# Optimization experiments

Measured on AMD Instinct MI355X. Metric: run time of the kernel, lower is better.

## Reference

```python
import jax, jax.numpy as jnp
import numpy as np
from jax import lax

BN_EPS = 1e-5


def _gcn_layer(X, edge_index, W, sW, sb, gamma, beta):
    # X: (B, T, V, Fin). Self-loop linear + per-edge message + scatter-add.
    H = X @ sW + sb  # (B, T, V, Hd)
    src = edge_index[:, 0]
    dst = edge_index[:, 1]
    msgs = X[:, :, src, :] @ W  # (B, T, E, Hd) gather + GEMM
    H = H + jnp.zeros_like(H).at[:, :, dst, :].add(msgs)  # scatter-add over dst
    # BatchNorm1d applied per timestep in the torch loop -> stats over (B, V) per t
    mean = H.mean(axis=(0, 2), keepdims=True)
    var = H.var(axis=(0, 2), keepdims=True)  # biased var, as torch train-mode BN
    H = (H - mean) * lax.rsqrt(var + BN_EPS) * gamma + beta
    return jax.nn.relu(H)


def _conv_bn_relu(x, w, b, gamma, beta, dilation, padding):
    # x: (B, C, T), w: (O, I, K)
    y = lax.conv_general_dilated(x, w, window_strides=(1,),
                                 padding=[(padding, padding)],
                                 rhs_dilation=(dilation,),
                                 dimension_numbers=('NCH', 'OIH', 'NCH'))
    y = y + b[None, :, None]
    mean = y.mean(axis=(0, 2), keepdims=True)
    var = y.var(axis=(0, 2), keepdims=True)
    y = (y - mean) * lax.rsqrt(var + BN_EPS) * gamma[None, :, None] + beta[None, :, None]
    return jax.nn.relu(y)


def setup_inputs() -> dict:
    key = jax.random.key(0)
    ks = jax.random.split(key, 16)
    B, C, T, V, Hd, E, NC = 64, 3, 512, 25, 64, 48, 60
    s = 0.05
    inp = {
        'X': jax.random.normal(ks[0], (B, C, T, V), jnp.float32),
        'edge_index': jax.random.randint(ks[1], (E, 2), 0, V, jnp.int32),
        'W1': jax.random.normal(ks[2], (C, Hd), jnp.float32) * s,
        's1W': jax.random.normal(ks[3], (C, Hd), jnp.float32) * s,
        's1b': jax.random.normal(ks[4], (Hd,), jnp.float32) * s,
        'g1': jnp.ones((Hd,), jnp.float32),
        'b1': jnp.zeros((Hd,), jnp.float32),
        'W2': jax.random.normal(ks[5], (Hd, Hd), jnp.float32) * s,
        's2W': jax.random.normal(ks[6], (Hd, Hd), jnp.float32) * s,
        's2b': jax.random.normal(ks[7], (Hd,), jnp.float32) * s,
        'g2': jnp.ones((Hd,), jnp.float32),
        'b2': jnp.zeros((Hd,), jnp.float32),
        'c1W': jax.random.normal(ks[8], (64, V * Hd, 3), jnp.float32) * s,
        'c1b': jax.random.normal(ks[9], (64,), jnp.float32) * s,
        'tg1': jnp.ones((64,), jnp.float32),
        'tb1': jnp.zeros((64,), jnp.float32),
        'c2W': jax.random.normal(ks[10], (128, 64, 3), jnp.float32) * s,
        'c2b': jax.random.normal(ks[11], (128,), jnp.float32) * s,
        'tg2': jnp.ones((128,), jnp.float32),
        'tb2': jnp.zeros((128,), jnp.float32),
        'fcW': jax.random.normal(ks[12], (128, NC), jnp.float32) * s,
        'fcb': jax.random.normal(ks[13], (NC,), jnp.float32) * s,
    }
    return inp


def reference(X, edge_index, W1, s1W, s1b, g1, b1, W2, s2W, s2b, g2, b2,
              c1W, c1b, tg1, tb1, c2W, c2b, tg2, tb2, fcW, fcb):
    B, C, T, V = X.shape
    Xt = jnp.transpose(X, (0, 2, 3, 1))  # (B, T, V, C)
    H = _gcn_layer(Xt, edge_index, W1, s1W, s1b, g1, b1)  # (B, T, V, Hd)
    H = _gcn_layer(H, edge_index, W2, s2W, s2b, g2, b2)   # (B, T, V, Hd)
    Hd = H.shape[-1]
    # permute(0,2,3,1).reshape(B, V*Hd, T)
    z = jnp.transpose(H, (0, 2, 3, 1)).reshape(B, V * Hd, T)
    z = _conv_bn_relu(z, c1W, c1b, tg1, tb1, dilation=1, padding=1)
    z = _conv_bn_relu(z, c2W, c2b, tg2, tb2, dilation=2, padding=2)
    z = z.mean(axis=2)  # (B, 128)
    return z @ fcW + fcb
```

## Files before the change

### kernel.cpp

```cpp
#include <hip/hip_runtime.h>
#include <hip/hip_bf16.h>
#include <cstddef>

using bf16 = __hip_bfloat16;
typedef __attribute__((ext_vector_type(4)))  short bf16x4;
typedef __attribute__((ext_vector_type(8)))  short bf16x8;
typedef __attribute__((ext_vector_type(4)))  float f32x4;
typedef __attribute__((ext_vector_type(16))) float f32x16;
typedef __attribute__((ext_vector_type(2)))  unsigned int uint32x2;
typedef __attribute__((ext_vector_type(4)))  unsigned int uint32x4;

#define B_   64
#define T_   512
#define V_   25
#define HD_  64
#define E_   48
#define NC_  60

__device__ __forceinline__ bf16  f2b(float x){ return __float2bfloat16(x); }
__device__ __forceinline__ unsigned short f2bits(float x){ return __builtin_bit_cast(unsigned short, f2b(x)); }
__device__ __forceinline__ float bits2f(unsigned short s){ return __builtin_bit_cast(float, ((unsigned)s)<<16); }
__device__ __forceinline__ unsigned cvtpk(float lo, float hi){
  unsigned r;
  asm("v_cvt_pk_bf16_f32 %0, %1, %2" : "=v"(r) : "v"(lo), "v"(hi));
  return r;
}
__device__ __forceinline__ short cvt1(float x){ return (short)(unsigned short)cvtpk(x, x); }

__global__ void k_csr(const int* __restrict__ ei, int* __restrict__ offs, int* __restrict__ lst)
{
  if(threadIdx.x == 0){
    int cnt[V_], pos[V_];
    for(int v=0;v<V_;v++) cnt[v]=0;
    for(int e=0;e<E_;e++) cnt[ei[2*e+1]]++;
    int off = 0;
    for(int v=0;v<V_;v++){ offs[v]=off; pos[v]=off; off+=cnt[v]; }
    offs[V_] = off;
    for(int e=0;e<E_;e++){ int d = ei[2*e+1]; lst[pos[d]++] = ei[2*e+0]; }
  }
}

__global__ void k_wt(const float* __restrict__ c1W, const float* __restrict__ c2W,
                     const float* __restrict__ s2W, const float* __restrict__ W2,
                     const float* __restrict__ s1W, const float* __restrict__ W1,
                     bf16* __restrict__ Wb, bf16* __restrict__ Wb2,
                     bf16* __restrict__ WbB, bf16* __restrict__ W6f)
{
  int i0 = blockIdx.x*blockDim.x + threadIdx.x, stride = gridDim.x*blockDim.x;
  for(int i = i0; i < 307200; i += stride){
    int hlo = i & 15, o = (i>>4)&63, kc = (i>>10)%12, v = i/12288;
    int ks = kc>>2, h = (kc&3)*16 + hlo;
    Wb[i] = f2b(c1W[(o*1600 + v*64 + h)*3 + ks]);
  }
  for(int i = i0; i < 24576; i += stride){
    int hlo = i & 15, o = (i>>4)&127, kc = i>>11;
    int ks = kc>>2, c = (kc&3)*16 + hlo;
    Wb2[i] = f2b(c2W[(o*64 + c)*3 + ks]);
  }
  for(int i = i0; i < 8192; i += stride){
    int j = i&7, l=(i>>3)&63, n=(i>>9)&3, kt=i>>11;
    int k = kt*32 + (l>>4)*8 + j;
    int h = n*16 + (l&15);
    float val = (k < 64) ? s2W[k*64 + h] : W2[(k-64)*64 + h];
    WbB[i] = f2b(val);
  }
  for(int i = i0; i < 2048; i += stride){
    int j = i&7, l=(i>>3)&63, n=(i>>9)&3;
    int k = (l>>4)*8 + j, h = n*16 + (l&15);
    float val = 0.f;
    if(k < 3) val = s1W[k*64 + h];
    else if(k < 6) val = W1[(k-3)*64 + h];
    W6f[i] = f2b(val);
  }
}

__global__ __launch_bounds__(512) void k_gcn1s(
    const float* __restrict__ X, const bf16* __restrict__ W6f,
    const int* __restrict__ offs, const int* __restrict__ lst, float* __restrict__ part)
{
  int tid = threadIdx.x, lane = tid & 63, wid = tid >> 6;
  int b = blockIdx.y, t0 = blockIdx.x*16;
  __shared__ short Z6[3200];
  __shared__ short Xs[1248];
  __shared__ float red[8192];
  __shared__ unsigned char soc[32], slc[48];

  bf16x8 w6[4];
  #pragma unroll
  for(int n=0;n<4;n++) w6[n] = *(const bf16x8*)&W6f[(n*64 + lane)*8];

  if(tid < V_+1) soc[tid] = (unsigned char)offs[tid];
  else if(tid >= 64 && tid < 64+E_) slc[tid-64] = (unsigned char)lst[tid-64];
  for(int i=tid; i<1248; i+=512){
    int c = i/416, r = i - c*416, tl = r/26, v = r - tl*26;
    short val = 0;
    if(v < 25) val = cvt1(X[((size_t)(b*3+c)*T_ + t0+tl)*V_ + v]);
    Xs[i] = val;
  }
  __syncthreads();
  if(tid < 400){
    int v = tid>>4, tl = tid&15, xb = tl*26;
    float a0=0.f, a1=0.f, a2=0.f;
    int e1 = soc[v+1];
    for(int e=soc[v]; e<e1; e++){
      int u = slc[e];
      a0 += bits2f((unsigned short)Xs[xb+u]);
      a1 += bits2f((unsigned short)Xs[416+xb+u]);
      a2 += bits2f((unsigned short)Xs[832+xb+u]);
    }
    unsigned p01 = cvtpk(a0, a1);
    bf16x8 z;
    z[0]=Xs[xb+v]; z[1]=Xs[416+xb+v]; z[2]=Xs[832+xb+v];
    z[3]=(short)p01; z[4]=(short)(p01>>16); z[5]=cvt1(a2);
    z[6]=0; z[7]=0;
    *(bf16x8*)&Z6[tid*8] = z;
  }
  __syncthreads();

  int l15 = lane & 15, tlb = (lane>>4)*4;
  f32x4 ssum[4] = {}, ssq[4] = {};
  #pragma unroll
  for(int vi=0; vi<4; vi++){
    int v = wid + vi*8;
    if(v < V_){
      bf16x8 af = {0,0,0,0,0,0,0,0};
      if(lane < 16) af = *(const bf16x8*)&Z6[(v*16 + lane)*8];
      #pragma unroll
      for(int n=0;n<4;n++){
        f32x4 c = {};
        c = __builtin_amdgcn_mfma_f32_16x16x32_bf16(af, w6[n], c, 0, 0, 0);
        #pragma unroll
        for(int j=0;j<4;j++){ float val = c[j]; ssum[n][j] += val; ssq[n][j] += val*val; }
      }
    }
  }
  #pragma unroll
  for(int n=0;n<4;n++)
    #pragma unroll
    for(int j=0;j<4;j++)
      red[wid*1024 + (tlb+j)*64 + n*16 + l15] = ssum[n][j];
  __syncthreads();
  size_t pb = ((size_t)blockIdx.x*64 + blockIdx.y)*2048;
  for(int i=tid; i<1024; i+=512){
    float s = 0.f;
    #pragma unroll
    for(int w=0;w<8;w++) s += red[w*1024 + i];
    __builtin_nontemporal_store(s, &part[pb + i]);
  }
  __syncthreads();
  #pragma unroll
  for(int n=0;n<4;n++)
    #pragma unroll
    for(int j=0;j<4;j++)
      red[wid*1024 + (tlb+j)*64 + n*16 + l15] = ssq[n][j];
  __syncthreads();
  for(int i=tid; i<1024; i+=512){
    float q = 0.f;
    #pragma unroll
    for(int w=0;w<8;w++) q += red[w*1024 + i];
    __builtin_nontemporal_store(q, &part[pb + 1024 + i]);
  }
}

__global__ void k_bnfin_th(const float* __restrict__ part,
                           const float* __restrict__ g, const float* __restrict__ bt,
                           float* __restrict__ scale, float* __restrict__ shift)
{
  int i = blockIdx.x*blockDim.x + threadIdx.x;
  if(i < T_*HD_){
    int h = i & 63, t = i >> 6, bx = t >> 4, tl = t & 15;
    const float* p = part + ((size_t)bx*64)*2048 + tl*64 + h;
    float s = 0.f, q = 0.f;
    for(int b=0;b<64;b++){ s += p[(size_t)b*2048]; q += p[(size_t)b*2048 + 1024]; }
    float m = s * (1.0f/1600.0f);
    float v = q * (1.0f/1600.0f) - m*m;
    float r = rsqrtf(fmaxf(v, 0.f) + 1e-5f);
    float sc = g[h]*r;
    scale[i] = sc;
    shift[i] = bt[h] - m*sc;
  }
}

__global__ __launch_bounds__(512,4) void k_gcn2(
    const float* __restrict__ X,
    const float* __restrict__ scale1, const float* __restrict__ shift1,
    const bf16* __restrict__ W6f, const bf16* __restrict__ WbB,
    const int* __restrict__ offs, const int* __restrict__ lst,
    unsigned char* __restrict__ Hout, float* __restrict__ part)
{
  int tid = threadIdx.x, lane = tid & 63, wid = tid >> 6;
  int b = blockIdx.y, t0 = blockIdx.x*16;
  __shared__ short Zs[400*72];
  __shared__ short WbBs[8192];
  __shared__ unsigned int pss[1024];
  __shared__ unsigned char soc[32], slc[48];
  short* Z6 = Zs;
  short* Xs = Zs + 3200;

  bf16x8 w6[4];
  #pragma unroll
  for(int n=0;n<4;n++) w6[n] = *(const bf16x8*)&W6f[(n*64 + lane)*8];

  if(tid < V_+1) soc[tid] = (unsigned char)offs[tid];
  else if(tid >= 64 && tid < 64+E_) slc[tid-64] = (unsigned char)lst[tid-64];
  for(int i=tid; i<1024; i+=512){
    pss[i] = ((unsigned)f2bits(shift1[t0*64+i])<<16) | f2bits(scale1[t0*64+i]);
    *(bf16x8*)&WbBs[i*8] = *(const bf16x8*)&WbB[i*8];
  }
  for(int i=tid; i<1248; i+=512){
    int c = i/416, r = i - c*416, tl = r/26, v = r - tl*26;
    short val = 0;
    if(v < 25) val = cvt1(X[((size_t)(b*3+c)*T_ + t0+tl)*V_ + v]);
    Xs[i] = val;
  }
  __syncthreads();

  if(tid < 400){
    int v = tid>>4, tl = tid&15, xb = tl*26;
    float a0=0.f, a1=0.f, a2=0.f;
    int e1 = soc[v+1];
    for(int e=soc[v]; e<e1; e++){
      int u = slc[e];
      a0 += bits2f((unsigned short)Xs[xb+u]);
      a1 += bits2f((unsigned short)Xs[416+xb+u]);
      a2 += bits2f((unsigned short)Xs[832+xb+u]);
    }
    unsigned p01 = cvtpk(a0, a1);
    bf16x8 z;
    z[0]=Xs[xb+v]; z[1]=Xs[416+xb+v]; z[2]=Xs[832+xb+v];
    z[3]=(short)p01; z[4]=(short)(p01>>16); z[5]=cvt1(a2);
    z[6]=0; z[7]=0;
    *(bf16x8*)&Z6[tid*8] = z;
  }
  __syncthreads();

  f32x4 c1f[4][4] = {};
  #pragma unroll
  for(int vi=0; vi<4; vi++){
    int v = wid + vi*8;
    if(v < V_){
      bf16x8 af = {0,0,0,0,0,0,0,0};
      if(lane < 16) af = *(const bf16x8*)&Z6[(v*16 + lane)*8];
      #pragma unroll
      for(int n=0;n<4;n++)
        c1f[vi][n] = __builtin_amdgcn_mfma_f32_16x16x32_bf16(af, w6[n], c1f[vi][n], 0, 0, 0);
    }
  }
  __syncthreads();

  int l15 = lane & 15, tlb = (lane>>4)*4;
  #pragma unroll
  for(int vi=0; vi<4; vi++){
    int v = wid + vi*8;
    if(v < V_){
      #pragma unroll
      for(int n=0;n<4;n++){
        float y[4];
        #pragma unroll
        for(int j=0;j<4;j++){
          unsigned u = pss[(tlb+j)*64 + n*16 + l15];
          y[j] = fmaxf(c1f[vi][n][j]*bits2f((unsigned short)(u&0xffffu)) + bits2f((unsigned short)(u>>16)), 0.f);
        }
        unsigned p01 = cvtpk(y[0], y[1]), p23 = cvtpk(y[2], y[3]);
        short* base = &Zs[(v*16 + tlb)*72 + n*16 + l15];
        base[0]   = (short)p01;  base[72]  = (short)(p01>>16);
        base[144] = (short)p23;  base[216] = (short)(p23>>16);
      }
    }
  }
  __syncthreads();

  int cg = (lane>>4)*8;
  f32x4 accs[4][4] = {};
  #pragma unroll
  for(int vi=0; vi<4; vi++){
    int v = wid + vi*8;
    if(v < V_){
      const short* rowp = &Zs[(v*16 + l15)*72 + cg];
      bf16x8 a0 = *(const bf16x8*)rowp;
      bf16x8 a1 = *(const bf16x8*)(rowp + 32);
      float s0[8]={0,0,0,0,0,0,0,0}, s1[8]={0,0,0,0,0,0,0,0};
      int e1 = soc[v+1];
      for(int e=soc[v]; e<e1; e++){
        int u = slc[e];
        const short* np = &Zs[(u*16 + l15)*72 + cg];
        bf16x8 n0 = *(const bf16x8*)np;
        bf16x8 n1 = *(const bf16x8*)(np + 32);
        #pragma unroll
        for(int j=0;j<8;j++){ s0[j] += bits2f((unsigned short)n0[j]); s1[j] += bits2f((unsigned short)n1[j]); }
      }
      uint32x4 ua2, ua3;
      #pragma unroll
      for(int j=0;j<4;j++){ ua2[j] = cvtpk(s0[2*j], s0[2*j+1]); ua3[j] = cvtpk(s1[2*j], s1[2*j+1]); }
      bf16x8 a2 = __builtin_bit_cast(bf16x8, ua2);
      bf16x8 a3 = __builtin_bit_cast(bf16x8, ua3);
      #pragma unroll
      for(int n=0;n<4;n++){
        bf16x8 b0 = *(const bf16x8*)&WbBs[(( 0+n)*64 + lane)*8];
        accs[vi][n] = __builtin_amdgcn_mfma_f32_16x16x32_bf16(a0, b0, accs[vi][n], 0, 0, 0);
        bf16x8 b1 = *(const bf16x8*)&WbBs[(( 4+n)*64 + lane)*8];
        accs[vi][n] = __builtin_amdgcn_mfma_f32_16x16x32_bf16(a1, b1, accs[vi][n], 0, 0, 0);
        bf16x8 b2 = *(const bf16x8*)&WbBs[(( 8+n)*64 + lane)*8];
        accs[vi][n] = __builtin_amdgcn_mfma_f32_16x16x32_bf16(a2, b2, accs[vi][n], 0, 0, 0);
        bf16x8 b3 = *(const bf16x8*)&WbBs[((12+n)*64 + lane)*8];
        accs[vi][n] = __builtin_amdgcn_mfma_f32_16x16x32_bf16(a3, b3, accs[vi][n], 0, 0, 0);
      }
    }
  }
  __syncthreads();

  f32x4 ssum[4] = {}, ssq[4] = {};
  #pragma unroll
  for(int vi=0; vi<4; vi++){
    int v = wid + vi*8;
    if(v < V_){
      #pragma unroll
      for(int n=0;n<4;n++){
        float val[4];
        #pragma unroll
        for(int j=0;j<4;j++){
          val[j] = accs[vi][n][j];
          ssum[n][j] += val[j]; ssq[n][j] += val[j]*val[j];
        }
        unsigned p01 = cvtpk(val[0], val[1]), p23 = cvtpk(val[2], val[3]);
        short* base = &Zs[(tlb*25 + v)*72 + n*16 + l15];
        base[0]    = (short)p01;  base[1800] = (short)(p01>>16);
        base[3600] = (short)p23;  base[5400] = (short)(p23>>16);
      }
    }
  }
  __syncthreads();

  unsigned char* hbout = Hout + ((size_t)b*T_ + t0)*V_*64;
  for(int c=tid; c<3200; c+=512){
    bf16x8 o = *(const bf16x8*)&Zs[(c>>3)*72 + (c&7)*8];
    float f[8];
    #pragma unroll
    for(int j=0;j<8;j++) f[j] = bits2f((unsigned short)o[j]);
    int w0 = 0, w1 = 0;
    w0 = __builtin_amdgcn_cvt_pk_fp8_f32(f[0], f[1], w0, false);
    w0 = __builtin_amdgcn_cvt_pk_fp8_f32(f[2], f[3], w0, true);
    w1 = __builtin_amdgcn_cvt_pk_fp8_f32(f[4], f[5], w1, false);
    w1 = __builtin_amdgcn_cvt_pk_fp8_f32(f[6], f[7], w1, true);
    uint32x2 st; st.x = (unsigned)w0; st.y = (unsigned)w1;
    __builtin_nontemporal_store(st, (uint32x2*)&hbout[(size_t)c*8]);
  }
  __syncthreads();

  float* red = (float*)Zs;
  size_t pb = ((size_t)blockIdx.x*64 + blockIdx.y)*2048;
  #pragma unroll
  for(int n=0;n<4;n++)
    #pragma unroll
    for(int j=0;j<4;j++)
      red[wid*1024 + (tlb+j)*64 + n*16 + l15] = ssum[n][j];
  __syncthreads();
  for(int i=tid; i<1024; i+=512){
    float s = 0.f;
    #pragma unroll
    for(int w=0;w<8;w++) s += red[w*1024 + i];
    __builtin_nontemporal_store(s, &part[pb + i]);
  }
  __syncthreads();
  #pragma unroll
  for(int n=0;n<4;n++)
    #pragma unroll
    for(int j=0;j<4;j++)
      red[wid*1024 + (tlb+j)*64 + n*16 + l15] = ssq[n][j];
  __syncthreads();
  for(int i=tid; i<1024; i+=512){
    float q = 0.f;
    #pragma unroll
    for(int w=0;w<8;w++) q += red[w*1024 + i];
    __builtin_nontemporal_store(q, &part[pb + 1024 + i]);
  }
}

__device__ __forceinline__ uint32x2 loadH8(const unsigned char* H, int b, int v, int t0, int s){
  int ti = s>>3, h0 = (s&7)*8, t = t0-1+ti;
  uint32x2 r; r.x = 0u; r.y = 0u;
  if(t >= 0 && t < T_) r = *(const uint32x2*)&H[(((size_t)b*T_+t)*V_ + v)*HD_ + h0];
  return r;
}

__device__ __forceinline__ void xform_store(short* zbuf, const unsigned int* sshf, int s, uint32x2 raw){
  int ti = s>>3, h0 = (s&7)*8;
  uint4 u0 = *(const uint4*)&sshf[ti*64 + h0];
  uint4 u1 = *(const uint4*)&sshf[ti*64 + h0 + 4];
  unsigned int uu[8] = {u0.x,u0.y,u0.z,u0.w,u1.x,u1.y,u1.z,u1.w};
  float x[8];
  x[0] = __builtin_amdgcn_cvt_f32_fp8((int)raw.x, 0);
  x[1] = __builtin_amdgcn_cvt_f32_fp8((int)raw.x, 1);
  x[2] = __builtin_amdgcn_cvt_f32_fp8((int)raw.x, 2);
  x[3] = __builtin_amdgcn_cvt_f32_fp8((int)raw.x, 3);
  x[4] = __builtin_amdgcn_cvt_f32_fp8((int)raw.y, 0);
  x[5] = __builtin_amdgcn_cvt_f32_fp8((int)raw.y, 1);
  x[6] = __builtin_amdgcn_cvt_f32_fp8((int)raw.y, 2);
  x[7] = __builtin_amdgcn_cvt_f32_fp8((int)raw.y, 3);
  float r[8];
  #pragma unroll
  for(int j=0;j<8;j++){
    float scl = bits2f((unsigned short)(uu[j] & 0xffffu));
    float shf = bits2f((unsigned short)(uu[j] >> 16));
    r[j] = fmaxf(x[j]*scl + shf, 0.f);
  }
  uint32x4 u;
  #pragma unroll
  for(int j=0;j<4;j++) u[j] = cvtpk(r[2*j], r[2*j+1]);
  *(uint32x4*)&zbuf[ti*72 + h0] = u;
}

__global__ __launch_bounds__(256) void k_conv1(
    const unsigned char* __restrict__ H, const float* __restrict__ scale2, const float* __restrict__ shift2,
    const bf16* __restrict__ Wb, bf16* __restrict__ C1b, float* __restrict__ cpart1)
{
  int b = blockIdx.y, t0 = blockIdx.x*32, tid = threadIdx.x;
  int lane = tid & 63, w = tid >> 6;
  __shared__ unsigned int sshf[34*64];
  __shared__ short zs[2][2][34*72];

  for(int i = tid; i < 34*64; i += 256){
    int ti = i>>6, h = i&63, t = t0-1+ti;
    unsigned int u = 0;
    if(t >= 0 && t < T_){
      u = ((unsigned)f2bits(shift2[t*64+h])<<16) | f2bits(scale2[t*64+h]);
    }
    sshf[i] = u;
  }
  __syncthreads();

  {
    uint32x2 a0 = loadH8(H,b,0,t0,tid);
    uint32x2 b0 = loadH8(H,b,13,t0,tid);
    uint32x2 a1, b1; a1.x=a1.y=b1.x=b1.y=0u;
    if(tid<16){ a1 = loadH8(H,b,0,t0,tid+256); b1 = loadH8(H,b,13,t0,tid+256); }
    xform_store(&zs[0][0][0], sshf, tid, a0);
    xform_store(&zs[1][0][0], sshf, tid, b0);
    if(tid<16){ xform_store(&zs[0][0][0], sshf, tid+256, a1); xform_store(&zs[1][0][0], sshf, tid+256, b1); }
  }
  uint32x2 rA0 = loadH8(H,b,1,t0,tid), rB0 = loadH8(H,b,14,t0,tid);
  uint32x2 rA1, rB1; rA1.x=rA1.y=rB1.x=rB1.y=0u;
  if(tid<16){ rA1 = loadH8(H,b,1,t0,tid+256); rB1 = loadH8(H,b,14,t0,tid+256); }
  __syncthreads();

  int g = w >> 1;
  int o0 = (w & 1)*32;
  int vbase = g ? 13 : 0, nv = g ? 12 : 13;
  f32x16 acc = {};
  for(int i=0; i<13; i++){
    uint32x2 nA0, nA1, nB0, nB1;
    nA0.x=nA0.y=nA1.x=nA1.y=nB0.x=nB0.y=nB1.x=nB1.y=0u;
    if(i+2 < 13){
      nA0 = loadH8(H,b,i+2,t0,tid);
      if(tid<16) nA1 = loadH8(H,b,i+2,t0,tid+256);
    }
    if(i+2 < 12){
      nB0 = loadH8(H,b,13+i+2,t0,tid);
      if(tid<16) nB1 = loadH8(H,b,13+i+2,t0,tid+256);
    }
    if(i < nv){
      int v = vbase + i;
      const short* zbuf = &zs[g][i&1][0];
      #pragma unroll
      for(int kc=0; kc<12; kc++){
        int ks = kc>>2;
        bf16x8 af = *(const bf16x8*)&Wb[((v*12+kc)*64 + o0 + (lane&31))*16 + (lane>>5)*8];
        int row = (lane&31) + ks;
        int col = (kc&3)*16 + (lane>>5)*8;
        bf16x8 bfr = *(const bf16x8*)&zbuf[row*72 + col];
        acc = __builtin_amdgcn_mfma_f32_32x32x16_bf16(af, bfr, acc, 0, 0, 0);
      }
    }
    if(i+1 < 13){
      xform_store(&zs[0][(i+1)&1][0], sshf, tid, rA0);
      if(tid<16) xform_store(&zs[0][(i+1)&1][0], sshf, tid+256, rA1);
    }
    if(i+1 < 12){
      xform_store(&zs[1][(i+1)&1][0], sshf, tid, rB0);
      if(tid<16) xform_store(&zs[1][(i+1)&1][0], sshf, tid+256, rB1);
    }
    rA0=nA0; rA1=nA1; rB0=nB0; rB1=nB1;
    __syncthreads();
  }

  float* redB = (float*)&zs[0][0][0];
  short* Cs   = &zs[0][0][0] + 4224;
  if(g == 1){
    #pragma unroll
    for(int r=0;r<16;r++){
      int ol = (r&3) + 8*(r>>2) + 4*(lane>>5);
      redB[(w&1)*1056 + ol*33 + (lane&31)] = acc[r];
    }
  }
  __syncthreads();
  if(g == 0){
    #pragma unroll
    for(int r=0;r<16;r++){
      int ol = (r&3) + 8*(r>>2) + 4*(lane>>5);
      float val = acc[r] + redB[(w&1)*1056 + ol*33 + (lane&31)];
      Cs[((w&1)*32 + ol)*32 + (lane&31)] = cvt1(val);
    }
  }
  __syncthreads();

  {
    int o = tid>>2, tseg = (tid&3)*8;
    bf16x8 row = *(const bf16x8*)&Cs[o*32 + tseg];
    *(bf16x8*)&C1b[((size_t)b*64 + o)*T_ + t0 + tseg] = row;
  }
  if(tid < 64){
    float s = 0.f, q = 0.f;
    for(int t=0;t<32;t++){
      float v = bits2f((unsigned short)Cs[tid*32 + t]);
      s += v; q += v*v;
    }
    size_t pb = ((size_t)blockIdx.y*16 + blockIdx.x)*128;
    cpart1[pb + tid] = s;
    cpart1[pb + 64 + tid] = q;
  }
}

__global__ __launch_bounds__(256) void k_redch(const float* __restrict__ cpart,
    const float* __restrict__ g, const float* __restrict__ bt,
    float* __restrict__ scale, float* __restrict__ shift, int nch, int nblk, float inv_count)
{
  int o = blockIdx.x, tid = threadIdx.x;
  float s = 0.f, q = 0.f;
  for(int blk=tid; blk<nblk; blk+=256){
    s += cpart[(size_t)blk*2*nch + o];
    q += cpart[(size_t)blk*2*nch + nch + o];
  }
  for(int off=32; off; off>>=1){ s += __shfl_down(s, off); q += __shfl_down(q, off); }
  __shared__ float rs[4], rq[4];
  if((tid&63)==0){ rs[tid>>6]=s; rq[tid>>6]=q; }
  __syncthreads();
  if(tid==0){
    s = rs[0]+rs[1]+rs[2]+rs[3]; q = rq[0]+rq[1]+rq[2]+rq[3];
    float m = s*inv_count;
    float v = q*inv_count - m*m;
    float r = rsqrtf(fmaxf(v, 0.f) + 1e-5f);
    float sc = g[o]*r;
    scale[o] = sc; shift[o] = bt[o] - m*sc;
  }
}

__global__ __launch_bounds__(256) void k_conv2(
    const bf16* __restrict__ C1b, const float* __restrict__ scale3, const float* __restrict__ shift3,
    const bf16* __restrict__ Wb2, short* __restrict__ C2b, float* __restrict__ cpart)
{
  int b = blockIdx.y, t0 = blockIdx.x*64, tid = threadIdx.x;
  int lane = tid & 63, w = tid >> 6;
  __shared__ short zT[68*72];
  __shared__ float scl[64], shf[64];
  __shared__ float rpart[4][16][2][2];
  if(tid < 64){ scl[tid]=scale3[tid]; shf[tid]=shift3[tid]; }
  __syncthreads();
  for(int i=tid; i<4352; i+=256){
    int c = i/68, r = i%68, t = t0 - 2 + r;
    float val = 0.f;
    if(t >= 0 && t < T_) val = fmaxf(bits2f((unsigned short)__builtin_bit_cast(short, C1b[((size_t)b*64+c)*T_ + t]))*scl[c] + shf[c], 0.f);
    zT[r*72 + c] = cvt1(val);
  }
  __syncthreads();
  int o0 = w*32;
  float sr[16], qr[16];
  #pragma unroll
  for(int r=0;r<16;r++){ sr[r]=0.f; qr[r]=0.f; }
  #pragma unroll
  for(int tt=0; tt<2; tt++){
    int twv = tt*32;
    f32x16 acc = {};
    #pragma unroll
    for(int kc=0; kc<12; kc++){
      bf16x8 af = *(const bf16x8*)&Wb2[((kc*128) + o0 + (lane&31))*16 + (lane>>5)*8];
      bf16x8 bfr = *(const bf16x8*)&zT[(twv + (lane&31) + 2*(kc>>2))*72 + (kc&3)*16 + (lane>>5)*8];
      acc = __builtin_amdgcn_mfma_f32_32x32x16_bf16(af, bfr, acc, 0, 0, 0);
    }
    int t = t0 + twv + (lane&31);
    #pragma unroll
    for(int r=0;r<16;r++){
      int o = o0 + (r&3) + 8*(r>>2) + 4*(lane>>5);
      float y = acc[r];
      C2b[((size_t)b*128 + o)*T_ + t] = cvt1(y);
      sr[r] += y; qr[r] += y*y;
    }
  }
  #pragma unroll
  for(int r=0;r<16;r++){
    float s = sr[r], q = qr[r];
    #pragma unroll
    for(int m=1;m<=16;m<<=1){ s += __shfl_xor(s, m); q += __shfl_xor(q, m); }
    if((lane&31)==0){ rpart[w][r][lane>>5][0]=s; rpart[w][r][lane>>5][1]=q; }
  }
  __syncthreads();
  if(tid < 128){
    int wv = tid>>5, r = (tid>>1)&15, hf = tid&1;
    int o = wv*32 + (r&3) + 8*(r>>2) + 4*hf;
    size_t pb = ((size_t)(blockIdx.y*8 + blockIdx.x))*256;
    cpart[pb + o]       = rpart[wv][r][hf][0];
    cpart[pb + 128 + o] = rpart[wv][r][hf][1];
  }
}

__global__ __launch_bounds__(256) void k_head(
    const short* __restrict__ C2b, const float* __restrict__ scale4, const float* __restrict__ shift4,
    const float* __restrict__ fcW, const float* __restrict__ fcb, float* __restrict__ out)
{
  int b = blockIdx.x, tid = threadIdx.x;
  __shared__ float mean[128];
  __shared__ float ms[256];
  int ch = tid >> 1, p = tid & 1;
  float scl = scale4[ch], shf = shift4[ch];
  const short* src = C2b + ((size_t)b*128 + ch)*T_ + p*256;
  float s = 0.f;
  for(int i=0;i<32;i++){
    bf16x8 v8 = *(const bf16x8*)&src[i*8];
    #pragma unroll
    for(int j=0;j<8;j++) s += fmaxf(bits2f((unsigned short)v8[j])*scl + shf, 0.f);
  }
  ms[tid] = s;
  __syncthreads();
  if(tid < 128) mean[tid] = (ms[2*tid] + ms[2*tid+1]) * (1.0f/512.0f);
  __syncthreads();
  if(tid < NC_){
    float acc = fcb[tid];
    for(int c=0;c<128;c++) acc += mean[c]*fcW[c*NC_ + tid];
    out[b*NC_ + tid] = acc;
  }
}

extern "C" void kernel_launch(void* const* d_in, const int* in_sizes, int n_in,
                              void* d_out, int out_size, void* d_ws, size_t ws_size,
                              hipStream_t stream)
{
  const float* X   = (const float*)d_in[0];
  const int*   ei  = (const int*)  d_in[1];
  const float* W1  = (const float*)d_in[2];
  const float* s1W = (const float*)d_in[3];
  const float* g1  = (const float*)d_in[5];
  const float* b1  = (const float*)d_in[6];
  const float* W2  = (const float*)d_in[7];
  const float* s2W = (const float*)d_in[8];
  const float* g2  = (const float*)d_in[10];
  const float* b2  = (const float*)d_in[11];
  const float* c1W = (const float*)d_in[12];
  const float* tg1 = (const float*)d_in[14];
  const float* tb1 = (const float*)d_in[15];
  const float* c2W = (const float*)d_in[16];
  const float* tg2 = (const float*)d_in[18];
  const float* tb2 = (const float*)d_in[19];
  const float* fcW = (const float*)d_in[20];
  const float* fcb = (const float*)d_in[21];

  char* ws = (char*)d_ws;
  unsigned char* H = (unsigned char*)(ws);
  bf16*  C1b    = (bf16*) (ws + 104857600);
  float* cpart1 = (float*)(ws + 109051904);
  float* cpart2 = (float*)(ws + 109576192);
  float* part   = (float*)(ws + 113246208);
  short* C2b    = (short*)part;
  bf16*  Wb     = (bf16*) (ws + 130023424);
  bf16*  Wb2    = (bf16*) (ws + 131252224);
  bf16*  WbB    = (bf16*) (ws + 131350528);
  float* stats  = (float*)(ws + 131366912);
  bf16*  W6f    = (bf16*) (stats);
  float* scale1 = stats + 131456; float* shift1 = scale1 + 32768;
  float* scale2 = shift1 + 32768; float* shift2 = scale2 + 32768;
  float* scale3 = shift2 + 32768; float* shift3 = scale3 + 64;
  float* scale4 = shift3 + 64;    float* shift4 = scale4 + 128;
  int* csr_off = (int*)(shift4 + 128);
  int* csr_lst = csr_off + 32;

  k_csr<<<1, 64, 0, stream>>>(ei, csr_off, csr_lst);
  k_wt<<<256, 256, 0, stream>>>(c1W, c2W, s2W, W2, s1W, W1, Wb, Wb2, WbB, W6f);

  k_gcn1s<<<dim3(T_/16, B_), 512, 0, stream>>>(X, W6f, csr_off, csr_lst, part);
  k_bnfin_th<<<128, 256, 0, stream>>>(part, g1, b1, scale1, shift1);
  k_gcn2<<<dim3(T_/16, B_), 512, 0, stream>>>(X, scale1, shift1, W6f, WbB, csr_off, csr_lst, H, part);
  k_bnfin_th<<<128, 256, 0, stream>>>(part, g2, b2, scale2, shift2);
  k_conv1<<<dim3(16, B_), 256, 0, stream>>>(H, scale2, shift2, Wb, C1b, cpart1);
  k_redch<<<64, 256, 0, stream>>>(cpart1, tg1, tb1, scale3, shift3, 64, 1024, 1.0f/32768.0f);
  k_conv2<<<dim3(8, B_), 256, 0, stream>>>(C1b, scale3, shift3, Wb2, C2b, cpart2);
  k_redch<<<128, 256, 0, stream>>>(cpart2, tg2, tb2, scale4, shift4, 128, 512, 1.0f/32768.0f);
  k_head<<<B_, 256, 0, stream>>>(C2b, scale4, shift4, fcW, fcb, (float*)d_out);
}
```

Before: 212.1 us.

## Compute GCN layer-1 BN stats from input moments instead of full GEMM outputs

```diff
diff --git a/kernel.cpp b/kernel.cpp
--- a/kernel.cpp
+++ b/kernel.cpp
@@ -20,6 +20,7 @@
 __device__ __forceinline__ bf16  f2b(float x){ return __float2bfloat16(x); }
 __device__ __forceinline__ unsigned short f2bits(float x){ return __builtin_bit_cast(unsigned short, f2b(x)); }
 __device__ __forceinline__ float bits2f(unsigned short s){ return __builtin_bit_cast(float, ((unsigned)s)<<16); }
+__device__ __forceinline__ float rbf(float x){ return bits2f(f2bits(x)); }
 __device__ __forceinline__ unsigned cvtpk(float lo, float hi){
   unsigned r;
   asm("v_cvt_pk_bf16_f32 %0, %1, %2" : "=v"(r) : "v"(lo), "v"(hi));
@@ -27,9 +28,16 @@
 }
 __device__ __forceinline__ short cvt1(float x){ return (short)(unsigned short)cvtpk(x, x); }
 
-__global__ void k_csr(const int* __restrict__ ei, int* __restrict__ offs, int* __restrict__ lst)
-{
-  if(threadIdx.x == 0){
+__global__ void k_wt(const float* __restrict__ c1W, const float* __restrict__ c2W,
+                     const float* __restrict__ s2W, const float* __restrict__ W2,
+                     const float* __restrict__ s1W, const float* __restrict__ W1,
+                     const int* __restrict__ ei,
+                     bf16* __restrict__ Wb, bf16* __restrict__ Wb2,
+                     bf16* __restrict__ WbB, bf16* __restrict__ W6f,
+                     int* __restrict__ offs, int* __restrict__ lst)
+{
+  int i0 = blockIdx.x*blockDim.x + threadIdx.x, stride = gridDim.x*blockDim.x;
+  if(blockIdx.x == 0 && threadIdx.x == 0){
     int cnt[V_], pos[V_];
     for(int v=0;v<V_;v++) cnt[v]=0;
     for(int e=0;e<E_;e++) cnt[ei[2*e+1]]++;
@@ -38,15 +46,6 @@
     offs[V_] = off;
     for(int e=0;e<E_;e++){ int d = ei[2*e+1]; lst[pos[d]++] = ei[2*e+0]; }
   }
-}
-
-__global__ void k_wt(const float* __restrict__ c1W, const float* __restrict__ c2W,
-                     const float* __restrict__ s2W, const float* __restrict__ W2,
-                     const float* __restrict__ s1W, const float* __restrict__ W1,
-                     bf16* __restrict__ Wb, bf16* __restrict__ Wb2,
-                     bf16* __restrict__ WbB, bf16* __restrict__ W6f)
-{
-  int i0 = blockIdx.x*blockDim.x + threadIdx.x, stride = gridDim.x*blockDim.x;
   for(int i = i0; i < 307200; i += stride){
     int hlo = i & 15, o = (i>>4)&63, kc = (i>>10)%12, v = i/12288;
     int ks = kc>>2, h = (kc&3)*16 + hlo;
@@ -74,20 +73,16 @@
   }
 }
 
-__global__ __launch_bounds__(512) void k_gcn1s(
-    const float* __restrict__ X, const bf16* __restrict__ W6f,
-    const int* __restrict__ offs, const int* __restrict__ lst, float* __restrict__ part)
-{
-  int tid = threadIdx.x, lane = tid & 63, wid = tid >> 6;
+__global__ __launch_bounds__(512) void k_stats1(
+    const float* __restrict__ X,
+    const int* __restrict__ offs, const int* __restrict__ lst,
+    float* __restrict__ gpart)
+{
+  int tid = threadIdx.x;
   int b = blockIdx.y, t0 = blockIdx.x*16;
+  __shared__ short Xs[1248];
   __shared__ short Z6[3200];
-  __shared__ short Xs[1248];
-  __shared__ float red[8192];
   __shared__ unsigned char soc[32], slc[48];
-
-  bf16x8 w6[4];
-  #pragma unroll
-  for(int n=0;n<4;n++) w6[n] = *(const bf16x8*)&W6f[(n*64 + lane)*8];
 
   if(tid < V_+1) soc[tid] = (unsigned char)offs[tid];
   else if(tid >= 64 && tid < 64+E_) slc[tid-64] = (unsigned char)lst[tid-64];
@@ -117,49 +112,73 @@
   }
   __syncthreads();
 
-  int l15 = lane & 15, tlb = (lane>>4)*4;
-  f32x4 ssum[4] = {}, ssq[4] = {};
-  #pragma unroll
-  for(int vi=0; vi<4; vi++){
-    int v = wid + vi*8;
-    if(v < V_){
-      bf16x8 af = {0,0,0,0,0,0,0,0};
-      if(lane < 16) af = *(const bf16x8*)&Z6[(v*16 + lane)*8];
-      #pragma unroll
-      for(int n=0;n<4;n++){
-        f32x4 c = {};
-        c = __builtin_amdgcn_mfma_f32_16x16x32_bf16(af, w6[n], c, 0, 0, 0);
-        #pragma unroll
-        for(int j=0;j<4;j++){ float val = c[j]; ssum[n][j] += val; ssq[n][j] += val*val; }
-      }
-    }
-  }
-  #pragma unroll
-  for(int n=0;n<4;n++)
-    #pragma unroll
-    for(int j=0;j<4;j++)
-      red[wid*1024 + (tlb+j)*64 + n*16 + l15] = ssum[n][j];
-  __syncthreads();
-  size_t pb = ((size_t)blockIdx.x*64 + blockIdx.y)*2048;
-  for(int i=tid; i<1024; i+=512){
+  int t = tid>>5, item = tid&31;
+  if(item < 27){
+    int k = item, kk = -1;
+    if(item >= 6){
+      int r = item - 6; k = 0;
+      while(r >= 6-k){ r -= 6-k; k++; }
+      kk = k + r;
+    }
+    float acc = 0.f;
+    for(int v=0;v<25;v++){
+      const short* z = &Z6[(v*16 + t)*8];
+      float a = bits2f((unsigned short)z[k]);
+      if(kk < 0) acc += a;
+      else acc += a * bits2f((unsigned short)z[kk]);
+    }
+    gpart[((size_t)blockIdx.x*64 + b)*432 + t*27 + item] = acc;
+  }
+}
+
+__global__ __launch_bounds__(256) void k_bnfin1(
+    const float* __restrict__ gpart,
+    const float* __restrict__ s1W, const float* __restrict__ W1,
+    const float* __restrict__ g, const float* __restrict__ bt,
+    float* __restrict__ scale, float* __restrict__ shift)
+{
+  int tid = threadIdx.x;
+  int t0 = blockIdx.x*4;
+  int tx = t0 >> 4, tlb = t0 & 15;
+  __shared__ float SM[4][27];
+  __shared__ float Wsh[6][64];
+  for(int i=tid; i<108; i+=256){
+    int tl = i/27, item = i%27;
     float s = 0.f;
-    #pragma unroll
-    for(int w=0;w<8;w++) s += red[w*1024 + i];
-    __builtin_nontemporal_store(s, &part[pb + i]);
-  }
-  __syncthreads();
-  #pragma unroll
-  for(int n=0;n<4;n++)
-    #pragma unroll
-    for(int j=0;j<4;j++)
-      red[wid*1024 + (tlb+j)*64 + n*16 + l15] = ssq[n][j];
-  __syncthreads();
-  for(int i=tid; i<1024; i+=512){
-    float q = 0.f;
-    #pragma unroll
-    for(int w=0;w<8;w++) q += red[w*1024 + i];
-    __builtin_nontemporal_store(q, &part[pb + 1024 + i]);
-  }
+    for(int b=0;b<64;b++)
+      s += gpart[((size_t)tx*64 + b)*432 + (tlb+tl)*27 + item];
+    SM[tl][item] = s;
+  }
+  for(int i=tid; i<384; i+=256){
+    int k = i>>6, h = i&63;
+    float w = (k<3) ? s1W[k*64+h] : W1[(k-3)*64+h];
+    Wsh[k][h] = rbf(w);
+  }
+  __syncthreads();
+  int tl = tid>>6, h = tid&63;
+  float w[6];
+  #pragma unroll
+  for(int k=0;k<6;k++) w[k] = Wsh[k][h];
+  float lin = 0.f;
+  #pragma unroll
+  for(int k=0;k<6;k++) lin += w[k]*SM[tl][k];
+  float qq = 0.f;
+  int idx = 6;
+  #pragma unroll
+  for(int k=0;k<6;k++){
+    #pragma unroll 6
+    for(int kk=k;kk<6;kk++){
+      float c = w[k]*w[kk];
+      if(kk != k) c += c;
+      qq += c*SM[tl][idx++];
+    }
+  }
+  float m = lin * (1.0f/1600.0f);
+  float v = qq * (1.0f/1600.0f) - m*m;
+  float r = rsqrtf(fmaxf(v, 0.f) + 1e-5f);
+  float sc = g[h]*r;
+  scale[(t0+tl)*64 + h] = sc;
+  shift[(t0+tl)*64 + h] = bt[h] - m*sc;
 }
 
 __global__ void k_bnfin_th(const float* __restrict__ part,
@@ -658,6 +677,7 @@
   float* cpart1 = (float*)(ws + 109051904);
   float* cpart2 = (float*)(ws + 109576192);
   float* part   = (float*)(ws + 113246208);
+  float* gpart  = part;
   short* C2b    = (short*)part;
   bf16*  Wb     = (bf16*) (ws + 130023424);
   bf16*  Wb2    = (bf16*) (ws + 131252224);
@@ -671,11 +691,10 @@
   int* csr_off = (int*)(shift4 + 128);
   int* csr_lst = csr_off + 32;
 
-  k_csr<<<1, 64, 0, stream>>>(ei, csr_off, csr_lst);
-  k_wt<<<256, 256, 0, stream>>>(c1W, c2W, s2W, W2, s1W, W1, Wb, Wb2, WbB, W6f);
-
-  k_gcn1s<<<dim3(T_/16, B_), 512, 0, stream>>>(X, W6f, csr_off, csr_lst, part);
-  k_bnfin_th<<<128, 256, 0, stream>>>(part, g1, b1, scale1, shift1);
+  k_wt<<<256, 256, 0, stream>>>(c1W, c2W, s2W, W2, s1W, W1, ei, Wb, Wb2, WbB, W6f, csr_off, csr_lst);
+
+  k_stats1<<<dim3(T_/16, B_), 512, 0, stream>>>(X, csr_off, csr_lst, gpart);
+  k_bnfin1<<<128, 256, 0, stream>>>(gpart, s1W, W1, g1, b1, scale1, shift1);
   k_gcn2<<<dim3(T_/16, B_), 512, 0, stream>>>(X, scale1, shift1, W6f, WbB, csr_off, csr_lst, H, part);
   k_bnfin_th<<<128, 256, 0, stream>>>(part, g2, b2, scale2, shift2);
   k_conv1<<<dim3(16, B_), 256, 0, stream>>>(H, scale2, shift2, Wb, C1b, cpart1);
```

Measured after the change: 201.9 us. 1.05x faster.
